# Performance work log

Hardware: AMD Instinct MI355X
Metric: run time of the kernel (lower is better)

Reference implementation:

```python
import jax, jax.numpy as jnp
import numpy as np
from jax import lax

K = 9  # 3x3 kernel points


def _gather(feat, iy, ix):
    """feat: [B,C,H,W]; iy,ix: [B,K,H,W] int32. Zero padding outside bounds.
    Returns [B,C,K,H,W]."""
    B, C, H, W = feat.shape
    valid = ((iy >= 0) & (iy < H) & (ix >= 0) & (ix < W))
    iyc = jnp.clip(iy, 0, H - 1)
    ixc = jnp.clip(ix, 0, W - 1)
    flat = (iyc * W + ixc).reshape(B, 1, -1)            # [B,1,K*H*W]
    g = jnp.take_along_axis(feat.reshape(B, C, H * W), flat, axis=2)
    g = g.reshape(B, C, K, H, W)
    return g * valid[:, None].astype(feat.dtype)


def _bilinear(feat, ys, xs):
    """feat: [B,C,H,W]; ys,xs: [B,K,H,W] float sampling coords -> [B,C,K,H,W]."""
    y0 = jnp.floor(ys)
    x0 = jnp.floor(xs)
    wy = (ys - y0)[:, None]
    wx = (xs - x0)[:, None]
    y0i = y0.astype(jnp.int32)
    x0i = x0.astype(jnp.int32)
    y1i = y0i + 1
    x1i = x0i + 1
    v00 = _gather(feat, y0i, x0i)
    v01 = _gather(feat, y0i, x1i)
    v10 = _gather(feat, y1i, x0i)
    v11 = _gather(feat, y1i, x1i)
    return (v00 * (1 - wy) * (1 - wx) + v01 * (1 - wy) * wx
            + v10 * wy * (1 - wx) + v11 * wy * wx)


def _deform_layer(x, w_off, b_off, w, b, dilation=1):
    """Modulated deformable 3x3 conv, stride 1, padding=dilation (same size)."""
    B, C, H, W = x.shape
    # offset/mask conv (regular 3x3 conv, same padding)
    om = lax.conv_general_dilated(
        x, w_off, window_strides=(1, 1),
        padding=[(dilation, dilation), (dilation, dilation)],
        rhs_dilation=(dilation, dilation),
        dimension_numbers=('NCHW', 'OIHW', 'NCHW')) + b_off[None, :, None, None]
    off = om[:, :2 * K].reshape(B, K, 2, H, W)   # (dy, dx) per kernel point
    mask = jax.nn.sigmoid(om[:, 2 * K:])         # [B,K,H,W]
    dy = off[:, :, 0]
    dx = off[:, :, 1]
    # base kernel grid offsets (-d, 0, +d)
    ky, kx = jnp.meshgrid(jnp.arange(3), jnp.arange(3), indexing='ij')
    base_y = ((ky.reshape(-1) - 1) * dilation).astype(x.dtype)   # [K]
    base_x = ((kx.reshape(-1) - 1) * dilation).astype(x.dtype)
    gy = jnp.arange(H, dtype=x.dtype)
    gx = jnp.arange(W, dtype=x.dtype)
    ys = gy[None, None, :, None] + base_y[None, :, None, None] + dy  # [B,K,H,W]
    xs = gx[None, None, None, :] + base_x[None, :, None, None] + dx
    sampled = _bilinear(x, ys, xs) * mask[:, None]   # [B,C,K,H,W]
    wk = w.reshape(w.shape[0], w.shape[1], K)        # [O,I,K]
    out = jnp.einsum('bikhw,oik->bohw', sampled, wk) + b[None, :, None, None]
    return out


def setup_inputs() -> dict:
    key = jax.random.key(0)
    ks = jax.random.split(key, 16)
    B, C, H, W = 4, 256, 64, 64
    O = 256
    inp = {'x': jax.random.normal(ks[0], (B, C, H, W), jnp.float32)}
    chans = [(C, C), (C, O), (O, O)]  # layer i==num_layers-2 maps in->out
    for i, (ci, co) in enumerate(chans):
        k = jax.random.split(ks[i + 1], 4)
        # offset conv: 27 = 3*K channels (18 offsets + 9 masks); small init
        inp[f'w_off{i}'] = jax.random.normal(k[0], (3 * K, ci, 3, 3), jnp.float32) * 0.01
        inp[f'b_off{i}'] = jnp.zeros((3 * K,), jnp.float32)
        # deform conv weight: kaiming normal, fan_in = ci*K
        std = np.sqrt(2.0 / (ci * K)).astype(np.float32)
        inp[f'w{i}'] = jax.random.normal(k[1], (co, ci, 3, 3), jnp.float32) * std
        inp[f'b{i}'] = jnp.zeros((co,), jnp.float32)
    return inp


def reference(x, w_off0, b_off0, w0, b0, w_off1, b_off1, w1, b1,
              w_off2, b_off2, w2, b2):
    params = [(w_off0, b_off0, w0, b0),
              (w_off1, b_off1, w1, b1),
              (w_off2, b_off2, w2, b2)]
    for (wo, bo, w, b) in params:
        x = jax.nn.relu(_deform_layer(x, wo, bo, w, b, dilation=1))
    return x
```

## Files before the change

kernel.cpp:

```cpp
#include <hip/hip_runtime.h>
#include <math.h>

#define Bn 4
#define Cn 256
#define Hn 64
#define Wn 64
#define On 256
#define HWn 4096
#define Pn 16384
#define Kc 2304

#define LGKM0 0xc07f

typedef _Float16 half8 __attribute__((ext_vector_type(8)));
typedef float floatx4 __attribute__((ext_vector_type(4)));

__global__ void k_transpose_f2h(const float* __restrict__ in, _Float16* __restrict__ out,
                                int R, int Cc) {
  __shared__ float tile[32][33];
  int b = blockIdx.z;
  int c0 = blockIdx.x * 32, r0 = blockIdx.y * 32;
  const float* ib = in + (size_t)b * R * Cc;
  _Float16* ob = out + (size_t)b * R * Cc;
  int tx = threadIdx.x, ty = threadIdx.y;
#pragma unroll
  for (int i = 0; i < 32; i += 8)
    tile[ty + i][tx] = ib[(size_t)(r0 + ty + i) * Cc + (c0 + tx)];
  __syncthreads();
#pragma unroll
  for (int i = 0; i < 32; i += 8)
    ob[(size_t)(c0 + ty + i) * R + (r0 + tx)] = (_Float16)tile[tx][ty + i];
}

__global__ void k_transpose(const float* __restrict__ in, float* __restrict__ out,
                            int R, int Cc) {
  __shared__ float tile[32][33];
  int b = blockIdx.z;
  int c0 = blockIdx.x * 32, r0 = blockIdx.y * 32;
  const float* ib = in + (size_t)b * R * Cc;
  float* ob = out + (size_t)b * R * Cc;
  int tx = threadIdx.x, ty = threadIdx.y;
#pragma unroll
  for (int i = 0; i < 32; i += 8)
    tile[ty + i][tx] = ib[(size_t)(r0 + ty + i) * Cc + (c0 + tx)];
  __syncthreads();
#pragma unroll
  for (int i = 0; i < 32; i += 8)
    ob[(size_t)(c0 + ty + i) * R + (r0 + tx)] = tile[tx][ty + i];
}

__global__ void k_wt_pack(const float* __restrict__ w, _Float16* __restrict__ wtp) {
  int n = blockIdx.x;
  int ci = threadIdx.x;
  int g = n >> 4, col = n & 15;
  int cq = ci >> 6;
  int kk = ci & 63;
  int kq = kk >> 5;
  int k32 = kk & 31;
  int quad = k32 >> 3;
  int e = k32 & 7;
  const float* src = w + (size_t)n * 2304 + (size_t)ci * 9;
#pragma unroll
  for (int t = 0; t < 9; ++t) {
    int c = t * 4 + cq;
    size_t dst = ((size_t)((c * 16 + g) * 2 + kq)) * 512 + (quad * 16 + col) * 8 + e;
    wtp[dst] = (_Float16)src[t];
  }
}

__global__ void k_wt_off_pack(const float* __restrict__ w, _Float16* __restrict__ wbop) {
  int n = blockIdx.x;
  int ci = threadIdx.x;
  int g = n >> 4, col = n & 15;
  int cw = ci >> 6;
  int r = ci & 63;
  int kq = r >> 5;
  int r2 = r & 31;
  int quad = r2 >> 3;
  int e = r2 & 7;
#pragma unroll
  for (int t = 0; t < 9; ++t) {
    int c = t * 4 + cw;
    size_t dst = ((size_t)((c * 2 + g) * 2 + kq)) * 512 + (quad * 16 + col) * 8 + e;
    wbop[dst] = (n < 27) ? (_Float16)w[((size_t)n * 256 + ci) * 9 + t] : (_Float16)0.f;
  }
}

__global__ __launch_bounds__(256, 4) void k_off_mfma(const _Float16* __restrict__ xh,
                                                     const _Float16* __restrict__ wbop,
                                                     const float* __restrict__ boff,
                                                     float* __restrict__ om) {
  __shared__ __align__(16) _Float16 Ao[2][32][72];
  __shared__ __align__(16) _Float16 Bo[2][2048];

  int p0 = blockIdx.x * 32;
  int tid = threadIdx.x;
  int lane = tid & 63;
  int wave = tid >> 6;
  int mg = wave >> 1;
  int ng = wave & 1;
  int quad = lane >> 4;
  int col = lane & 15;

  int ar = tid >> 3;
  int aci = (tid & 7) * 8;

  int p = p0 + ar;
  int bimg = p >> 12;
  int yx = p & 4095;
  int y = yx >> 6, x = yx & 63;

  half8 zero8;
#pragma unroll
  for (int e = 0; e < 8; ++e) zero8[e] = (_Float16)0.f;

  floatx4 acc = (floatx4){0.f, 0.f, 0.f, 0.f};

  half8 ga, gb;
  int abase = 0;
  bool avalid = false;

  {
    int sy = y - 1, sx = x - 1;
    avalid = (sy >= 0) & (sy < Hn) & (sx >= 0) & (sx < Wn);
    abase = (((bimg * Hn + (avalid ? sy : 0)) * Wn) + (avalid ? sx : 0)) * Cn;
    ga = zero8;
    if (avalid) ga = *(const half8*)(xh + (size_t)abase + aci);
    gb = *(const half8*)(wbop + (size_t)tid * 8);
  }

#pragma unroll
  for (int c = 0; c < 36; ++c) {
    int buf = c & 1;
    *(half8*)&Ao[buf][ar][aci] = ga;
    *(half8*)&Bo[buf][tid * 8] = gb;

    if (c < 35) {
      int cn = c + 1;
      int tn = cn >> 2;
      int cin = (cn & 3) * 64;
      if ((cn & 3) == 0) {
        int sy = y + tn / 3 - 1;
        int sx = x + tn % 3 - 1;
        avalid = (sy >= 0) & (sy < Hn) & (sx >= 0) & (sx < Wn);
        abase = (((bimg * Hn + (avalid ? sy : 0)) * Wn) + (avalid ? sx : 0)) * Cn;
      }
      ga = zero8;
      if (avalid) ga = *(const half8*)(xh + (size_t)abase + cin + aci);
      gb = *(const half8*)(wbop + (size_t)cn * 2048 + tid * 8);
    }

    __builtin_amdgcn_s_waitcnt(LGKM0);
    __builtin_amdgcn_s_barrier();

    half8 af[2], bf[2];
#pragma unroll
    for (int kq = 0; kq < 2; ++kq) {
      af[kq] = *(const half8*)&Ao[buf][mg * 16 + col][kq * 32 + quad * 8];
      bf[kq] = *(const half8*)&Bo[buf][(ng * 2 + kq) * 512 + lane * 8];
    }
#pragma unroll
    for (int kq = 0; kq < 2; ++kq)
      acc = __builtin_amdgcn_mfma_f32_16x16x32_f16(af[kq], bf[kq], acc, 0, 0, 0);
  }

  int n = ng * 16 + col;
  if (n < 27) {
    float bb = boff[n];
#pragma unroll
    for (int r = 0; r < 4; ++r) {
      int pp = p0 + mg * 16 + quad * 4 + r;
      om[(size_t)pp * 32 + n] = acc[r] + bb;
    }
  }
}

__global__ void k_coords(const float* __restrict__ om, float* __restrict__ samp) {
  int idx = blockIdx.x * 256 + threadIdx.x;
  int k = idx % 9;
  int p = idx / 9;
  int bimg = p >> 12;
  int yx = p & 4095;
  int y = yx >> 6, x = yx & 63;

  const float* o = om + (size_t)p * 32;
  float dy = o[2 * k];
  float dx = o[2 * k + 1];
  float m = 1.f / (1.f + expf(-o[18 + k]));

  float ys = (float)(y + k / 3 - 1) + dy;
  float xs = (float)(x + k % 3 - 1) + dx;
  float y0f = floorf(ys), x0f = floorf(xs);
  float wy = ys - y0f, wx = xs - x0f;
  int y0 = (int)y0f, x0 = (int)x0f;
  int y1 = y0 + 1, x1 = x0 + 1;

  bool vy0 = (y0 >= 0) & (y0 < Hn);
  bool vy1 = (y1 >= 0) & (y1 < Hn);
  bool vx0 = (x0 >= 0) & (x0 < Wn);
  bool vx1 = (x1 >= 0) & (x1 < Wn);
  int y0c = min(max(y0, 0), Hn - 1), y1c = min(max(y1, 0), Hn - 1);
  int x0c = min(max(x0, 0), Wn - 1), x1c = min(max(x1, 0), Wn - 1);

  int base = bimg * HWn;
  int o00 = (base + y0c * Wn + x0c) * Cn;
  int o01 = (base + y0c * Wn + x1c) * Cn;
  int o10 = (base + y1c * Wn + x0c) * Cn;
  int o11 = (base + y1c * Wn + x1c) * Cn;

  float w00 = (vy0 && vx0) ? m * (1.f - wy) * (1.f - wx) : 0.f;
  float w01 = (vy0 && vx1) ? m * (1.f - wy) * wx : 0.f;
  float w10 = (vy1 && vx0) ? m * wy * (1.f - wx) : 0.f;
  float w11 = (vy1 && vx1) ? m * wy * wx : 0.f;

  float* s = samp + (size_t)idx * 8;
  ((int*)s)[0] = o00; ((int*)s)[1] = o01; ((int*)s)[2] = o10; ((int*)s)[3] = o11;
  s[4] = w00; s[5] = w01; s[6] = w10; s[7] = w11;
}

__global__ __launch_bounds__(512, 2) void k_gemm_main(
    const _Float16* __restrict__ xh, const float* __restrict__ samp,
    const _Float16* __restrict__ wtp, const float* __restrict__ bias,
    _Float16* __restrict__ outh, float* __restrict__ outf) {
  __shared__ __align__(16) _Float16 As[2][64][72];
  __shared__ __align__(16) _Float16 Bs[2][16384];

  int p0 = blockIdx.x * 64;
  int tid = threadIdx.x;
  int lane = tid & 63;
  int wave = tid >> 6;
  int quad = lane >> 4;
  int col = lane & 15;
  int mw = wave >> 2;
  int nw = wave & 3;

  int ar = tid >> 3;
  int aci = (tid & 7) * 8;

  const float* smp = samp + (size_t)(p0 + ar) * 72;

  float bj[4];
#pragma unroll
  for (int j = 0; j < 4; ++j) bj[j] = bias[(nw * 4 + j) * 16 + col];

  floatx4 acc[2][4];
#pragma unroll
  for (int i = 0; i < 2; ++i)
#pragma unroll
    for (int j = 0; j < 4; ++j) acc[i][j] = (floatx4){0.f, 0.f, 0.f, 0.f};

  half8 g00, g01, g10, g11;
  half8 bst[4];
  int4 ofsS[2];
  float4 wvS[2];

  ofsS[0] = *(const int4*)(smp);
  wvS[0] = *(const float4*)(smp + 4);
  g00 = *(const half8*)(xh + (size_t)ofsS[0].x + aci);
  g01 = *(const half8*)(xh + (size_t)ofsS[0].y + aci);
  g10 = *(const half8*)(xh + (size_t)ofsS[0].z + aci);
  g11 = *(const half8*)(xh + (size_t)ofsS[0].w + aci);
#pragma unroll
  for (int q = 0; q < 4; ++q)
    bst[q] = *(const half8*)(wtp + (size_t)(q * 512 + tid) * 8);

#pragma unroll
  for (int c = 0; c < 36; ++c) {
    int buf = c & 1;
    int t = c >> 2;
    {
      float4 wv = wvS[t & 1];
      _Float16 h00 = (_Float16)wv.x, h01 = (_Float16)wv.y;
      _Float16 h10 = (_Float16)wv.z, h11 = (_Float16)wv.w;
      half8 r;
#pragma unroll
      for (int e = 0; e < 8; ++e)
        r[e] = g00[e] * h00 + g01[e] * h01 + g10[e] * h10 + g11[e] * h11;
      *(half8*)&As[buf][ar][aci] = r;
    }
#pragma unroll
    for (int q = 0; q < 4; ++q)
      *(half8*)&Bs[buf][(q * 512 + tid) * 8] = bst[q];

    if (c < 35) {
      int cn = c + 1;
      int tn = cn >> 2;
      int cin = (cn & 3) * 64;
      int4 ofs = ofsS[tn & 1];
      int ci = cin + aci;
      g00 = *(const half8*)(xh + (size_t)ofs.x + ci);
      g01 = *(const half8*)(xh + (size_t)ofs.y + ci);
      g10 = *(const half8*)(xh + (size_t)ofs.z + ci);
      g11 = *(const half8*)(xh + (size_t)ofs.w + ci);
      const _Float16* wsrc = wtp + (size_t)cn * 16384;
#pragma unroll
      for (int q = 0; q < 4; ++q)
        bst[q] = *(const half8*)(wsrc + (size_t)(q * 512 + tid) * 8);
    }
    if ((c & 3) == 0 && t + 1 <= 8) {
      int tnl = t + 1;
      ofsS[tnl & 1] = *(const int4*)(smp + tnl * 8);
      wvS[tnl & 1] = *(const float4*)(smp + tnl * 8 + 4);
    }

    __builtin_amdgcn_s_waitcnt(LGKM0);
    __builtin_amdgcn_s_barrier();

    half8 af[2][2];
#pragma unroll
    for (int kq = 0; kq < 2; ++kq)
#pragma unroll
      for (int i = 0; i < 2; ++i)
        af[kq][i] = *(const half8*)&As[buf][mw * 32 + i * 16 + col][kq * 32 + quad * 8];

    half8 bf[2][4];
#pragma unroll
    for (int kq = 0; kq < 2; ++kq)
#pragma unroll
      for (int j = 0; j < 4; ++j)
        bf[kq][j] = *(const half8*)&Bs[buf][((nw * 4 + j) * 2 + kq) * 512 + lane * 8];

#pragma unroll
    for (int kq = 0; kq < 2; ++kq)
#pragma unroll
      for (int i = 0; i < 2; ++i)
#pragma unroll
        for (int j = 0; j < 4; ++j)
          acc[i][j] = __builtin_amdgcn_mfma_f32_16x16x32_f16(
              af[kq][i], bf[kq][j], acc[i][j], 0, 0, 0);
  }

#pragma unroll
  for (int i = 0; i < 2; ++i)
#pragma unroll
    for (int j = 0; j < 4; ++j) {
      int n = (nw * 4 + j) * 16 + col;
#pragma unroll
      for (int r = 0; r < 4; ++r) {
        int p = p0 + mw * 32 + i * 16 + quad * 4 + r;
        float v = fmaxf(acc[i][j][r] + bj[j], 0.f);
        if (outf) outf[(size_t)p * On + n] = v;
        else outh[(size_t)p * On + n] = (_Float16)v;
      }
    }
}

extern "C" void kernel_launch(void* const* d_in, const int* in_sizes, int n_in,
                              void* d_out, int out_size, void* d_ws, size_t ws_size,
                              hipStream_t stream) {
  (void)in_sizes; (void)n_in; (void)out_size; (void)ws_size;
  const float* x = (const float*)d_in[0];

  _Float16* act0h = (_Float16*)d_ws;
  _Float16* act1h = act0h + (size_t)Pn * Cn;
  float* actf32   = (float*)(act1h + (size_t)Pn * Cn);
  float* om       = actf32 + (size_t)Pn * On;
  float* sampb    = om + (size_t)Pn * 32;
  _Float16* wbop  = (_Float16*)(sampb + (size_t)Pn * 9 * 8);
  _Float16* wtp   = wbop + (size_t)36 * 2048;

  dim3 tb(32, 8);
  k_transpose_f2h<<<dim3(HWn / 32, Cn / 32, Bn), tb, 0, stream>>>(x, act0h, Cn, HWn);

  _Float16* cur = act0h;
  _Float16* nxt = act1h;
  for (int l = 0; l < 3; ++l) {
    const float* w_off = (const float*)d_in[1 + l * 4];
    const float* b_off = (const float*)d_in[2 + l * 4];
    const float* w     = (const float*)d_in[3 + l * 4];
    const float* b     = (const float*)d_in[4 + l * 4];

    k_wt_off_pack<<<32, 256, 0, stream>>>(w_off, wbop);
    k_wt_pack<<<256, 256, 0, stream>>>(w, wtp);
    k_off_mfma<<<Pn / 32, 256, 0, stream>>>(cur, wbop, b_off, om);
    k_coords<<<(Pn * 9) / 256, 256, 0, stream>>>(om, sampb);
    k_gemm_main<<<Pn / 64, 512, 0, stream>>>(cur, sampb, wtp, b, nxt,
                                             (l == 2) ? actf32 : nullptr);
    _Float16* tswap = cur; cur = nxt; nxt = tswap;
  }
  k_transpose<<<dim3(On / 32, HWn / 32, Bn), tb, 0, stream>>>(actf32, (float*)d_out, HWn, On);
}
```

Before: 261.8 us.

## Fuse coord computation into offset conv, batch weight packing, write NCHW output directly

Folds the sampling-coordinate computation into the offset-conv MFMA kernel through a shared-memory tile, so the om buffer round-trip and one launch per layer go away. All six weight packings are merged into one upfront kernel that writes per-layer packed buffers, which removes six launches. The last GEMM stores float4 outputs straight into NCHW layout, eliminating the final transpose kernel and the fp32 intermediate buffer. The trade-offs are a strided epilogue store pattern and a longer tail in the offset kernel.

```diff
diff --git a/kernel.cpp b/kernel.cpp
--- a/kernel.cpp
+++ b/kernel.cpp
@@ -32,66 +32,60 @@
     ob[(size_t)(c0 + ty + i) * R + (r0 + tx)] = (_Float16)tile[tx][ty + i];
 }
 
-__global__ void k_transpose(const float* __restrict__ in, float* __restrict__ out,
-                            int R, int Cc) {
-  __shared__ float tile[32][33];
-  int b = blockIdx.z;
-  int c0 = blockIdx.x * 32, r0 = blockIdx.y * 32;
-  const float* ib = in + (size_t)b * R * Cc;
-  float* ob = out + (size_t)b * R * Cc;
-  int tx = threadIdx.x, ty = threadIdx.y;
-#pragma unroll
-  for (int i = 0; i < 32; i += 8)
-    tile[ty + i][tx] = ib[(size_t)(r0 + ty + i) * Cc + (c0 + tx)];
-  __syncthreads();
-#pragma unroll
-  for (int i = 0; i < 32; i += 8)
-    ob[(size_t)(c0 + ty + i) * R + (r0 + tx)] = tile[tx][ty + i];
-}
-
-__global__ void k_wt_pack(const float* __restrict__ w, _Float16* __restrict__ wtp) {
-  int n = blockIdx.x;
+__global__ void k_pack_all(const float* __restrict__ w0, const float* __restrict__ w1,
+                           const float* __restrict__ w2, const float* __restrict__ wo0,
+                           const float* __restrict__ wo1, const float* __restrict__ wo2,
+                           _Float16* __restrict__ wtp, _Float16* __restrict__ wbop) {
+  int bx = blockIdx.x;
   int ci = threadIdx.x;
-  int g = n >> 4, col = n & 15;
-  int cq = ci >> 6;
-  int kk = ci & 63;
-  int kq = kk >> 5;
-  int k32 = kk & 31;
-  int quad = k32 >> 3;
-  int e = k32 & 7;
-  const float* src = w + (size_t)n * 2304 + (size_t)ci * 9;
-#pragma unroll
-  for (int t = 0; t < 9; ++t) {
-    int c = t * 4 + cq;
-    size_t dst = ((size_t)((c * 16 + g) * 2 + kq)) * 512 + (quad * 16 + col) * 8 + e;
-    wtp[dst] = (_Float16)src[t];
-  }
-}
-
-__global__ void k_wt_off_pack(const float* __restrict__ w, _Float16* __restrict__ wbop) {
-  int n = blockIdx.x;
-  int ci = threadIdx.x;
-  int g = n >> 4, col = n & 15;
-  int cw = ci >> 6;
-  int r = ci & 63;
-  int kq = r >> 5;
-  int r2 = r & 31;
-  int quad = r2 >> 3;
-  int e = r2 & 7;
-#pragma unroll
-  for (int t = 0; t < 9; ++t) {
-    int c = t * 4 + cw;
-    size_t dst = ((size_t)((c * 2 + g) * 2 + kq)) * 512 + (quad * 16 + col) * 8 + e;
-    wbop[dst] = (n < 27) ? (_Float16)w[((size_t)n * 256 + ci) * 9 + t] : (_Float16)0.f;
+  if (bx < 768) {
+    int l = bx >> 8;
+    int n = bx & 255;
+    const float* w = (l == 0) ? w0 : (l == 1) ? w1 : w2;
+    _Float16* dst = wtp + (size_t)l * 256 * Kc;
+    int g = n >> 4, col = n & 15;
+    int cq = ci >> 6;
+    int kk = ci & 63;
+    int kq = kk >> 5;
+    int k32 = kk & 31;
+    int quad = k32 >> 3;
+    int e = k32 & 7;
+    const float* src = w + (size_t)n * 2304 + (size_t)ci * 9;
+#pragma unroll
+    for (int t = 0; t < 9; ++t) {
+      int c = t * 4 + cq;
+      size_t d = ((size_t)((c * 16 + g) * 2 + kq)) * 512 + (quad * 16 + col) * 8 + e;
+      dst[d] = (_Float16)src[t];
+    }
+  } else {
+    int b2 = bx - 768;
+    int l = b2 >> 5;
+    int n = b2 & 31;
+    const float* w = (l == 0) ? wo0 : (l == 1) ? wo1 : wo2;
+    _Float16* dst = wbop + (size_t)l * 36 * 2048;
+    int g = n >> 4, col = n & 15;
+    int cw = ci >> 6;
+    int r = ci & 63;
+    int kq = r >> 5;
+    int r2 = r & 31;
+    int quad = r2 >> 3;
+    int e = r2 & 7;
+#pragma unroll
+    for (int t = 0; t < 9; ++t) {
+      int c = t * 4 + cw;
+      size_t d = ((size_t)((c * 2 + g) * 2 + kq)) * 512 + (quad * 16 + col) * 8 + e;
+      dst[d] = (n < 27) ? (_Float16)w[((size_t)n * 256 + ci) * 9 + t] : (_Float16)0.f;
+    }
   }
 }
 
 __global__ __launch_bounds__(256, 4) void k_off_mfma(const _Float16* __restrict__ xh,
                                                      const _Float16* __restrict__ wbop,
                                                      const float* __restrict__ boff,
-                                                     float* __restrict__ om) {
+                                                     float* __restrict__ samp) {
   __shared__ __align__(16) _Float16 Ao[2][32][72];
   __shared__ __align__(16) _Float16 Bo[2][2048];
+  __shared__ float omS[32][33];
 
   int p0 = blockIdx.x * 32;
   int tid = threadIdx.x;
@@ -168,54 +162,52 @@
   if (n < 27) {
     float bb = boff[n];
 #pragma unroll
-    for (int r = 0; r < 4; ++r) {
-      int pp = p0 + mg * 16 + quad * 4 + r;
-      om[(size_t)pp * 32 + n] = acc[r] + bb;
-    }
-  }
-}
-
-__global__ void k_coords(const float* __restrict__ om, float* __restrict__ samp) {
-  int idx = blockIdx.x * 256 + threadIdx.x;
-  int k = idx % 9;
-  int p = idx / 9;
-  int bimg = p >> 12;
-  int yx = p & 4095;
-  int y = yx >> 6, x = yx & 63;
-
-  const float* o = om + (size_t)p * 32;
-  float dy = o[2 * k];
-  float dx = o[2 * k + 1];
-  float m = 1.f / (1.f + expf(-o[18 + k]));
-
-  float ys = (float)(y + k / 3 - 1) + dy;
-  float xs = (float)(x + k % 3 - 1) + dx;
-  float y0f = floorf(ys), x0f = floorf(xs);
-  float wy = ys - y0f, wx = xs - x0f;
-  int y0 = (int)y0f, x0 = (int)x0f;
-  int y1 = y0 + 1, x1 = x0 + 1;
-
-  bool vy0 = (y0 >= 0) & (y0 < Hn);
-  bool vy1 = (y1 >= 0) & (y1 < Hn);
-  bool vx0 = (x0 >= 0) & (x0 < Wn);
-  bool vx1 = (x1 >= 0) & (x1 < Wn);
-  int y0c = min(max(y0, 0), Hn - 1), y1c = min(max(y1, 0), Hn - 1);
-  int x0c = min(max(x0, 0), Wn - 1), x1c = min(max(x1, 0), Wn - 1);
-
-  int base = bimg * HWn;
-  int o00 = (base + y0c * Wn + x0c) * Cn;
-  int o01 = (base + y0c * Wn + x1c) * Cn;
-  int o10 = (base + y1c * Wn + x0c) * Cn;
-  int o11 = (base + y1c * Wn + x1c) * Cn;
-
-  float w00 = (vy0 && vx0) ? m * (1.f - wy) * (1.f - wx) : 0.f;
-  float w01 = (vy0 && vx1) ? m * (1.f - wy) * wx : 0.f;
-  float w10 = (vy1 && vx0) ? m * wy * (1.f - wx) : 0.f;
-  float w11 = (vy1 && vx1) ? m * wy * wx : 0.f;
-
-  float* s = samp + (size_t)idx * 8;
-  ((int*)s)[0] = o00; ((int*)s)[1] = o01; ((int*)s)[2] = o10; ((int*)s)[3] = o11;
-  s[4] = w00; s[5] = w01; s[6] = w10; s[7] = w11;
+    for (int r = 0; r < 4; ++r)
+      omS[mg * 16 + quad * 4 + r][n] = acc[r] + bb;
+  }
+  __syncthreads();
+
+  for (int e = tid; e < 288; e += 256) {
+    int lp = e / 9;
+    int k = e - lp * 9;
+    int pp = p0 + lp;
+    int bi = pp >> 12;
+    int pyx = pp & 4095;
+    int py = pyx >> 6, px = pyx & 63;
+
+    float dy = omS[lp][2 * k];
+    float dx = omS[lp][2 * k + 1];
+    float m = 1.f / (1.f + expf(-omS[lp][18 + k]));
+
+    float ys = (float)(py + k / 3 - 1) + dy;
+    float xs = (float)(px + k % 3 - 1) + dx;
+    float y0f = floorf(ys), x0f = floorf(xs);
+    float wy = ys - y0f, wx = xs - x0f;
+    int y0 = (int)y0f, x0 = (int)x0f;
+    int y1 = y0 + 1, x1 = x0 + 1;
+
+    bool vy0 = (y0 >= 0) & (y0 < Hn);
+    bool vy1 = (y1 >= 0) & (y1 < Hn);
+    bool vx0 = (x0 >= 0) & (x0 < Wn);
+    bool vx1 = (x1 >= 0) & (x1 < Wn);
+    int y0c = min(max(y0, 0), Hn - 1), y1c = min(max(y1, 0), Hn - 1);
+    int x0c = min(max(x0, 0), Wn - 1), x1c = min(max(x1, 0), Wn - 1);
+
+    int base = bi * HWn;
+    int o00 = (base + y0c * Wn + x0c) * Cn;
+    int o01 = (base + y0c * Wn + x1c) * Cn;
+    int o10 = (base + y1c * Wn + x0c) * Cn;
+    int o11 = (base + y1c * Wn + x1c) * Cn;
+
+    float w00 = (vy0 && vx0) ? m * (1.f - wy) * (1.f - wx) : 0.f;
+    float w01 = (vy0 && vx1) ? m * (1.f - wy) * wx : 0.f;
+    float w10 = (vy1 && vx0) ? m * wy * (1.f - wx) : 0.f;
+    float w11 = (vy1 && vx1) ? m * wy * wx : 0.f;
+
+    float* s = samp + (size_t)(pp * 9 + k) * 8;
+    ((int*)s)[0] = o00; ((int*)s)[1] = o01; ((int*)s)[2] = o10; ((int*)s)[3] = o11;
+    s[4] = w00; s[5] = w01; s[6] = w10; s[7] = w11;
+  }
 }
 
 __global__ __launch_bounds__(512, 2) void k_gemm_main(
@@ -335,12 +327,23 @@
 #pragma unroll
     for (int j = 0; j < 4; ++j) {
       int n = (nw * 4 + j) * 16 + col;
-#pragma unroll
-      for (int r = 0; r < 4; ++r) {
-        int p = p0 + mw * 32 + i * 16 + quad * 4 + r;
-        float v = fmaxf(acc[i][j][r] + bj[j], 0.f);
-        if (outf) outf[(size_t)p * On + n] = v;
-        else outh[(size_t)p * On + n] = (_Float16)v;
+      if (outf) {
+        int pb = p0 + mw * 32 + i * 16 + quad * 4;
+        int bi = pb >> 12;
+        int yx = pb & 4095;
+        float4 v;
+        v.x = fmaxf(acc[i][j][0] + bj[j], 0.f);
+        v.y = fmaxf(acc[i][j][1] + bj[j], 0.f);
+        v.z = fmaxf(acc[i][j][2] + bj[j], 0.f);
+        v.w = fmaxf(acc[i][j][3] + bj[j], 0.f);
+        *(float4*)(outf + ((size_t)(bi * On + n)) * HWn + yx) = v;
+      } else {
+#pragma unroll
+        for (int r = 0; r < 4; ++r) {
+          int p = p0 + mw * 32 + i * 16 + quad * 4 + r;
+          float v = fmaxf(acc[i][j][r] + bj[j], 0.f);
+          outh[(size_t)p * On + n] = (_Float16)v;
+        }
       }
     }
 }
@@ -353,30 +356,26 @@
 
   _Float16* act0h = (_Float16*)d_ws;
   _Float16* act1h = act0h + (size_t)Pn * Cn;
-  float* actf32   = (float*)(act1h + (size_t)Pn * Cn);
-  float* om       = actf32 + (size_t)Pn * On;
-  float* sampb    = om + (size_t)Pn * 32;
+  float* sampb    = (float*)(act1h + (size_t)Pn * Cn);
   _Float16* wbop  = (_Float16*)(sampb + (size_t)Pn * 9 * 8);
-  _Float16* wtp   = wbop + (size_t)36 * 2048;
+  _Float16* wtp   = wbop + (size_t)3 * 36 * 2048;
 
   dim3 tb(32, 8);
   k_transpose_f2h<<<dim3(HWn / 32, Cn / 32, Bn), tb, 0, stream>>>(x, act0h, Cn, HWn);
+  k_pack_all<<<864, 256, 0, stream>>>(
+      (const float*)d_in[3], (const float*)d_in[7], (const float*)d_in[11],
+      (const float*)d_in[1], (const float*)d_in[5], (const float*)d_in[9],
+      wtp, wbop);
 
   _Float16* cur = act0h;
   _Float16* nxt = act1h;
   for (int l = 0; l < 3; ++l) {
-    const float* w_off = (const float*)d_in[1 + l * 4];
     const float* b_off = (const float*)d_in[2 + l * 4];
-    const float* w     = (const float*)d_in[3 + l * 4];
     const float* b     = (const float*)d_in[4 + l * 4];
 
-    k_wt_off_pack<<<32, 256, 0, stream>>>(w_off, wbop);
-    k_wt_pack<<<256, 256, 0, stream>>>(w, wtp);
-    k_off_mfma<<<Pn / 32, 256, 0, stream>>>(cur, wbop, b_off, om);
-    k_coords<<<(Pn * 9) / 256, 256, 0, stream>>>(om, sampb);
-    k_gemm_main<<<Pn / 64, 512, 0, stream>>>(cur, sampb, wtp, b, nxt,
-                                             (l == 2) ? actf32 : nullptr);
+    k_off_mfma<<<Pn / 32, 256, 0, stream>>>(cur, wbop + (size_t)l * 36 * 2048, b_off, sampb);
+    k_gemm_main<<<Pn / 64, 512, 0, stream>>>(cur, sampb, wtp + (size_t)l * 256 * Kc, b, nxt,
+                                             (l == 2) ? (float*)d_out : nullptr);
     _Float16* tswap = cur; cur = nxt; nxt = tswap;
   }
-  k_transpose<<<dim3(On / 32, HWn / 32, Bn), tb, 0, stream>>>(actf32, (float*)d_out, HWn, On);
-}
+}
```

Measured after the change: 240.4 us. -8.2%, faster.
